# Optimization experiments

Measured on AMD Instinct MI355X. Metric: run time of the kernel, lower is better.

The kernel has to match this reference:

```python
import jax, jax.numpy as jnp
import numpy as np
from jax import lax

VOCAB, EMB, RNN = 20000, 300, 512
B, NCLS, TWORDS = 64, 200, 8


def setup_inputs() -> dict:
    key = jax.random.key(0)
    ks = jax.random.split(key, 10)
    s = 0.05
    return {
        "sentence": jax.random.randint(ks[0], (B, NCLS, TWORDS), 0, VOCAB, dtype=jnp.int32),
        "word2vec": jax.random.normal(ks[1], (VOCAB, EMB), dtype=jnp.float32) * s,
        "W_ih1": jax.random.normal(ks[2], (4 * RNN, EMB), dtype=jnp.float32) * s,
        "W_hh1": jax.random.normal(ks[3], (4 * RNN, RNN), dtype=jnp.float32) * s,
        "b_ih1": jax.random.normal(ks[4], (4 * RNN,), dtype=jnp.float32) * s,
        "b_hh1": jax.random.normal(ks[5], (4 * RNN,), dtype=jnp.float32) * s,
        "W_ih2": jax.random.normal(ks[6], (4 * RNN, RNN), dtype=jnp.float32) * s,
        "W_hh2": jax.random.normal(ks[7], (4 * RNN, RNN), dtype=jnp.float32) * s,
        "b_ih2": jax.random.normal(ks[8], (4 * RNN,), dtype=jnp.float32) * s,
        "b_hh2": jax.random.normal(ks[9], (4 * RNN,), dtype=jnp.float32) * s,
    }


def _lstm_cell(x, h, c, W_ih, W_hh, b):
    # PyTorch LSTMCell gate order: i, f, g, o
    gates = x @ W_ih.T + h @ W_hh.T + b  # [BN, 4*RNN]
    i, f, g, o = jnp.split(gates, 4, axis=-1)
    c_new = jax.nn.sigmoid(f) * c + jax.nn.sigmoid(i) * jnp.tanh(g)
    h_new = jax.nn.sigmoid(o) * jnp.tanh(c_new)
    return h_new, c_new


def reference(sentence, word2vec, W_ih1, W_hh1, b_ih1, b_hh1, W_ih2, W_hh2, b_ih2, b_hh2):
    batch, num_class, max_words = sentence.shape
    bn = batch * num_class
    ids = sentence.reshape(bn, max_words)
    # embedding gather + tanh (dropout is identity in eval mode)
    emb = jnp.tanh(word2vec[ids])              # [BN, T, EMB]
    xs = jnp.swapaxes(emb, 0, 1)               # [T, BN, EMB]
    b1 = b_ih1 + b_hh1
    b2 = b_ih2 + b_hh2
    rnn = W_hh1.shape[1]
    zeros = jnp.zeros((bn, rnn), dtype=word2vec.dtype)
    init = (zeros, zeros, zeros, zeros)

    def step(carry, x):
        h1, c1, h2, c2 = carry
        h1, c1 = _lstm_cell(x, h1, c1, W_ih1, W_hh1, b1)
        h2, c2 = _lstm_cell(h1, h2, c2, W_ih2, W_hh2, b2)
        return (h1, c1, h2, c2), None

    (h1, c1, h2, c2), _ = lax.scan(step, init, xs)
    return h2.reshape(batch, num_class, rnn)
```

## Files before the change

### kernel.cpp

```cpp
#include <hip/hip_runtime.h>
#include <hip/hip_bf16.h>

#define BROWS  12800
#define TSTEPS 8
#define EMB    300
#define EMBP   320
#define RNN    512
#define NG     2048
#define K1     832
#define K2     1024
#define VOCAB  20000

typedef short bf16x8 __attribute__((ext_vector_type(8)));
typedef float f32x4  __attribute__((ext_vector_type(4)));
typedef __hip_bfloat16 bf16;

__device__ __forceinline__ float sigmoidf_(float x) { return 1.f / (1.f + __expf(-x)); }
__device__ __forceinline__ float tanhf_(float x)    { return 1.f - 2.f / (__expf(2.f * x) + 1.f); }

__device__ __forceinline__ void gl_lds16(const bf16* g, bf16* l) {
    __builtin_amdgcn_global_load_lds(
        (const __attribute__((address_space(1))) void*)g,
        (__attribute__((address_space(3))) void*)l,
        16, 0, 0);
}

__global__ void convert_weights(const float* __restrict__ Wih1, const float* __restrict__ Whh1,
                                const float* __restrict__ Wih2, const float* __restrict__ Whh2,
                                const float* __restrict__ bih1, const float* __restrict__ bhh1,
                                const float* __restrict__ bih2, const float* __restrict__ bhh2,
                                bf16* __restrict__ Wc1, bf16* __restrict__ Wc2,
                                float* __restrict__ Bp1, float* __restrict__ Bp2) {
    int idx = blockIdx.x * 256 + threadIdx.x;
    const int n1 = NG * K1;
    const int n2 = NG * K2;
    if (idx < n1) {
        int n = idx / K1, k = idx - n * K1;
        int on = ((n >> 4) & 3) * RNN + (n >> 6) * 16 + (n & 15);
        float v = 0.f;
        if (k < EMB)        v = Wih1[on * EMB + k];
        else if (k >= EMBP) v = Whh1[on * RNN + (k - EMBP)];
        Wc1[idx] = __float2bfloat16(v);
    }
    if (idx < n2) {
        int n = idx >> 10, k = idx & (K2 - 1);
        int on = ((n >> 4) & 3) * RNN + (n >> 6) * 16 + (n & 15);
        float v = (k < RNN) ? Wih2[on * RNN + k] : Whh2[on * RNN + (k - RNN)];
        Wc2[idx] = __float2bfloat16(v);
    }
    if (idx < NG) {
        int on = ((idx >> 4) & 3) * RNN + (idx >> 6) * 16 + (idx & 15);
        Bp1[idx] = bih1[on] + bhh1[on];
        Bp2[idx] = bih2[on] + bhh2[on];
    }
}

__global__ void tanh_w2v(const float* __restrict__ w2v, bf16* __restrict__ W2Vt) {
    int row = blockIdx.x;
    int col = threadIdx.x;
    float v = (col < EMB) ? tanhf_(w2v[row * EMB + col]) : 0.f;
    W2Vt[(size_t)row * EMBP + col] = __float2bfloat16(v);
}

#define BM 128
#define BN 128

__global__ __launch_bounds__(256, 4) void gemm_lstm(
        int role_base, int t,
        const bf16* __restrict__ W2Vt, const int* __restrict__ sent,
        const bf16* __restrict__ Asrc,
        bf16* __restrict__ hdst,
        const bf16* __restrict__ Wc1, const bf16* __restrict__ Wc2,
        const float* __restrict__ Bp1, const float* __restrict__ Bp2,
        float* __restrict__ cst1, float* __restrict__ cst2,
        float* __restrict__ outf, int en_out,
        int Kl1, int Kl2) {
    __shared__ __attribute__((aligned(16))) bf16 sA[BM * 64];
    __shared__ __attribute__((aligned(16))) bf16 sB[BN * 64];

    const int tid  = threadIdx.x;
    const int lane = tid & 63;
    const int wave = tid >> 6;
    const int wm   = wave >> 1, wn = wave & 1;
    const int bn   = blockIdx.x;
    const int bm   = blockIdx.y;
    const int role = blockIdx.z + role_base;

    const bf16*  W;  int ldw, Kl, ksplit, offh;
    const float* Bp; float* cst;
    if (role) { W = Wc1; ldw = K1; Kl = Kl1; ksplit = EMBP; offh = 0;   Bp = Bp1; cst = cst1; }
    else      { W = Wc2; ldw = K2; Kl = Kl2; ksplit = 0;    offh = RNN; Bp = Bp2; cst = cst2; }

    f32x4 acc[4][4];
#pragma unroll
    for (int i = 0; i < 4; ++i)
#pragma unroll
        for (int j = 0; j < 4; ++j)
#pragma unroll
            for (int r = 0; r < 4; ++r) acc[i][j][r] = 0.f;

    const int r = lane & 15, q = lane >> 4;

    int srow[4], scol[4];
#pragma unroll
    for (int c = 0; c < 4; ++c) {
        int ch = c * 256 + tid;
        srow[c] = ch >> 3;
        scol[c] = ((ch & 7) ^ (srow[c] & 7)) * 8;
    }

    int idv[4];
    if (role) {
#pragma unroll
        for (int c = 0; c < 4; ++c)
            idv[c] = sent[(size_t)(bm * BM + srow[c]) * TSTEPS + t];
    }

    const bf16* Wbase = W + (size_t)(bn * BN) * ldw;
    const bf16* Abase = Asrc + (size_t)(bm * BM) * K2;

    for (int kb = 0; kb < Kl; kb += 64) {
        const bool xreg = (kb < ksplit);
#pragma unroll
        for (int c = 0; c < 4; ++c) {
            int ch = c * 256 + tid;
            const bf16* alane = xreg
                ? W2Vt  + (size_t)idv[c] * EMBP + kb + scol[c]
                : Abase + (size_t)srow[c] * K2 + (kb - ksplit) + scol[c];
            gl_lds16(alane, &sA[ch * 8]);
            gl_lds16(Wbase + (size_t)srow[c] * ldw + kb + scol[c], &sB[ch * 8]);
        }
        __syncthreads();
#pragma unroll
        for (int kk = 0; kk < 64; kk += 32) {
            const int kc = kk >> 3;
            bf16x8 af[4], wf[4];
#pragma unroll
            for (int i = 0; i < 4; ++i)
                af[i] = *(const bf16x8*)(&sA[(wm * 64 + i * 16 + r) * 64 + (((q + kc) ^ (r & 7)) * 8)]);
#pragma unroll
            for (int j = 0; j < 4; ++j)
                wf[j] = *(const bf16x8*)(&sB[(wn * 64 + j * 16 + r) * 64 + (((q + kc) ^ (r & 7)) * 8)]);
#pragma unroll
            for (int i = 0; i < 4; ++i)
#pragma unroll
                for (int j = 0; j < 4; ++j)
                    acc[i][j] = __builtin_amdgcn_mfma_f32_16x16x32_bf16(
                        af[i], wf[j], acc[i][j], 0, 0, 0);
        }
        __syncthreads();
    }

    const int colb = bn * BN + wn * 64;
    const int u    = (2 * bn + wn) * 16 + r;
    const float bi = Bp[colb + r];
    const float bf = Bp[colb + 16 + r];
    const float bg = Bp[colb + 32 + r];
    const float bo = Bp[colb + 48 + r];

    float cc[4][4];
#pragma unroll
    for (int i = 0; i < 4; ++i)
#pragma unroll
        for (int rr = 0; rr < 4; ++rr) {
            int row = bm * BM + wm * 64 + i * 16 + q * 4 + rr;
            cc[i][rr] = cst[(size_t)row * RNN + u];
        }

#define HLD 40
#pragma unroll
    for (int i = 0; i < 4; ++i) {
#pragma unroll
        for (int rr = 0; rr < 4; ++rr) {
            int rowl = wm * 64 + i * 16 + q * 4 + rr;
            int row  = bm * BM + rowl;
            size_t cidx = (size_t)row * RNN + u;
            float gi = acc[i][0][rr] + bi;
            float gf = acc[i][1][rr] + bf;
            float gg = acc[i][2][rr] + bg;
            float go = acc[i][3][rr] + bo;
            float cn = sigmoidf_(gf) * cc[i][rr] + sigmoidf_(gi) * tanhf_(gg);
            float h  = sigmoidf_(go) * tanhf_(cn);
            cst[cidx] = cn;
            if (en_out) outf[cidx] = h;
            sA[rowl * HLD + wn * 16 + r] = __float2bfloat16(h);
        }
    }
    __syncthreads();

#pragma unroll
    for (int half = 0; half < 2; ++half) {
        int t2   = half * 256 + tid;
        int rowl = t2 >> 2;
        int c8   = (t2 & 3) * 8;
        uint4 v  = *(const uint4*)&sA[rowl * HLD + c8];
        int row  = bm * BM + rowl;
        int gcol = bn * 32 + c8;
        *(uint4*)&hdst[(size_t)row * K2 + offh + gcol] = v;
    }
#undef HLD
}

extern "C" void kernel_launch(void* const* d_in, const int* in_sizes, int n_in,
                              void* d_out, int out_size, void* d_ws, size_t ws_size,
                              hipStream_t stream) {
    (void)in_sizes; (void)n_in; (void)out_size; (void)ws_size;
    const int*   sent = (const int*)d_in[0];
    const float* w2v  = (const float*)d_in[1];
    const float* Wih1 = (const float*)d_in[2];
    const float* Whh1 = (const float*)d_in[3];
    const float* bih1 = (const float*)d_in[4];
    const float* bhh1 = (const float*)d_in[5];
    const float* Wih2 = (const float*)d_in[6];
    const float* Whh2 = (const float*)d_in[7];
    const float* bih2 = (const float*)d_in[8];
    const float* bhh2 = (const float*)d_in[9];
    float* out = (float*)d_out;

    char* ws = (char*)d_ws;
    float* c1   = (float*)(ws);
    float* c2   = (float*)(ws + 26214400);
    bf16*  A2[2];
    A2[0] = (bf16*)(ws + 52428800);
    A2[1] = (bf16*)(ws + 78643200);
    bf16*  W2Vt = (bf16*) (ws + 104857600);
    bf16*  Wc1  = (bf16*) (ws + 117657600);
    bf16*  Wc2  = (bf16*) (ws + 121065472);
    float* Bp1  = (float*)(ws + 125259776);
    float* Bp2  = (float*)(ws + 125267968);

    hipMemsetAsync(ws, 0, 52428800, stream);

    convert_weights<<<dim3((NG * K2 + 255) / 256), dim3(256), 0, stream>>>(
        Wih1, Whh1, Wih2, Whh2, bih1, bhh1, bih2, bhh2, Wc1, Wc2, Bp1, Bp2);

    tanh_w2v<<<dim3(VOCAB), dim3(EMBP), 0, stream>>>(w2v, W2Vt);

    gemm_lstm<<<dim3(NG / BN, BROWS / BM, 1), dim3(256), 0, stream>>>(
        1, 0, W2Vt, sent,
        A2[1] , A2[0],
        Wc1, Wc2, Bp1, Bp2, c1, c2,
        (float*)nullptr, 0,
        EMBP , 0 );

    for (int s = 1; s <= 7; ++s) {
        gemm_lstm<<<dim3(NG / BN, BROWS / BM, 2), dim3(256), 0, stream>>>(
            0, s, W2Vt, sent,
            A2[(s - 1) & 1], A2[s & 1],
            Wc1, Wc2, Bp1, Bp2, c1, c2,
            (float*)nullptr, 0,
            K1 , (s == 1) ? RNN : K2 );
    }

    gemm_lstm<<<dim3(NG / BN, BROWS / BM, 1), dim3(256), 0, stream>>>(
        0, 0 , W2Vt, sent,
        A2[1], A2[0],
        Wc1, Wc2, Bp1, Bp2, c1, c2,
        out, 1,
        K1 , K2 );
}
```

Before: 1.037 ms.

## Remap blocks XCD-aware, use pointer-increment K loop, skip c-state memset

Workgroup IDs are remapped so that consecutive logical tiles are grouped by raw&7, placing tiles that share weight and activation rows on the same XCD for better L2 reuse. The K loop is split into an embedding-gather phase and a hidden-state phase with running pointers, which removes the per-iteration branch and address recomputation. The 50MB workspace memset is dropped, and the first step of each layer treats the cell state as zero through a flag instead of reading it. The remap relies on the hardcoded grid size of 1600 tiles per role.

New measurement: 1.011 ms. -2.5%, faster.

```diff
diff --git a/kernel.cpp b/kernel.cpp
--- a/kernel.cpp
+++ b/kernel.cpp
@@ -74,7 +74,7 @@
         const float* __restrict__ Bp1, const float* __restrict__ Bp2,
         float* __restrict__ cst1, float* __restrict__ cst2,
         float* __restrict__ outf, int en_out,
-        int Kl1, int Kl2) {
+        int Kl1, int Kl2, int cz1, int cz2) {
     __shared__ __attribute__((aligned(16))) bf16 sA[BM * 64];
     __shared__ __attribute__((aligned(16))) bf16 sB[BN * 64];
 
@@ -82,14 +82,21 @@
     const int lane = tid & 63;
     const int wave = tid >> 6;
     const int wm   = wave >> 1, wn = wave & 1;
-    const int bn   = blockIdx.x;
-    const int bm   = blockIdx.y;
-    const int role = blockIdx.z + role_base;
-
-    const bf16*  W;  int ldw, Kl, ksplit, offh;
+
+    const int zdim  = (int)gridDim.z;
+    const int chunk = (zdim * 1600) >> 3;
+    const int raw   = blockIdx.x + (blockIdx.y << 4) + blockIdx.z * 1600;
+    const int lgc   = (raw & 7) * chunk + (raw >> 3);
+    int role, rem;
+    if (zdim == 2) { role = (lgc >= 1600) ? 1 : 0; rem = lgc - (role ? 1600 : 0); }
+    else           { role = role_base;             rem = lgc; }
+    const int bn = rem & 15;
+    const int bm = rem >> 4;
+
+    const bf16*  W;  int ldw, Kl, ksplit, offh, czero;
     const float* Bp; float* cst;
-    if (role) { W = Wc1; ldw = K1; Kl = Kl1; ksplit = EMBP; offh = 0;   Bp = Bp1; cst = cst1; }
-    else      { W = Wc2; ldw = K2; Kl = Kl2; ksplit = 0;    offh = RNN; Bp = Bp2; cst = cst2; }
+    if (role) { W = Wc1; ldw = K1; Kl = Kl1; ksplit = EMBP; offh = 0;   Bp = Bp1; cst = cst1; czero = cz1; }
+    else      { W = Wc2; ldw = K2; Kl = Kl2; ksplit = 0;    offh = RNN; Bp = Bp2; cst = cst2; czero = cz2; }
 
     f32x4 acc[4][4];
 #pragma unroll
@@ -109,31 +116,37 @@
         scol[c] = ((ch & 7) ^ (srow[c] & 7)) * 8;
     }
 
-    int idv[4];
-    if (role) {
-#pragma unroll
-        for (int c = 0; c < 4; ++c)
-            idv[c] = sent[(size_t)(bm * BM + srow[c]) * TSTEPS + t];
-    }
-
     const bf16* Wbase = W + (size_t)(bn * BN) * ldw;
     const bf16* Abase = Asrc + (size_t)(bm * BM) * K2;
 
-    for (int kb = 0; kb < Kl; kb += 64) {
-        const bool xreg = (kb < ksplit);
+    const bf16* ap[4];
+    const bf16* wp[4];
+#pragma unroll
+    for (int c = 0; c < 4; ++c)
+        wp[c] = Wbase + (size_t)srow[c] * ldw + scol[c];
+    if (role) {
 #pragma unroll
         for (int c = 0; c < 4; ++c) {
-            int ch = c * 256 + tid;
-            const bf16* alane = xreg
-                ? W2Vt  + (size_t)idv[c] * EMBP + kb + scol[c]
-                : Abase + (size_t)srow[c] * K2 + (kb - ksplit) + scol[c];
-            gl_lds16(alane, &sA[ch * 8]);
-            gl_lds16(Wbase + (size_t)srow[c] * ldw + kb + scol[c], &sB[ch * 8]);
+            int id = sent[(size_t)(bm * BM + srow[c]) * TSTEPS + t];
+            ap[c] = W2Vt + (size_t)id * EMBP + scol[c];
+        }
+    } else {
+#pragma unroll
+        for (int c = 0; c < 4; ++c)
+            ap[c] = Abase + (size_t)srow[c] * K2 + scol[c];
+    }
+
+    auto tile = [&]() {
+#pragma unroll
+        for (int c = 0; c < 4; ++c) {
+            gl_lds16(ap[c], &sA[(c * 256 + tid) * 8]);
+            gl_lds16(wp[c], &sB[(c * 256 + tid) * 8]);
+            ap[c] += 64; wp[c] += 64;
         }
         __syncthreads();
 #pragma unroll
-        for (int kk = 0; kk < 64; kk += 32) {
-            const int kc = kk >> 3;
+        for (int kk = 0; kk < 2; ++kk) {
+            const int kc = kk << 2;
             bf16x8 af[4], wf[4];
 #pragma unroll
             for (int i = 0; i < 4; ++i)
@@ -149,7 +162,17 @@
                         af[i], wf[j], acc[i][j], 0, 0, 0);
         }
         __syncthreads();
-    }
+    };
+
+    const int ntx = ksplit >> 6;
+    const int nth = (Kl - ksplit) >> 6;
+    for (int tt = 0; tt < ntx; ++tt) tile();
+    if (role) {
+#pragma unroll
+        for (int c = 0; c < 4; ++c)
+            ap[c] = Abase + (size_t)srow[c] * K2 + scol[c];
+    }
+    for (int tt = 0; tt < nth; ++tt) tile();
 
     const int colb = bn * BN + wn * 64;
     const int u    = (2 * bn + wn) * 16 + r;
@@ -159,13 +182,20 @@
     const float bo = Bp[colb + 48 + r];
 
     float cc[4][4];
-#pragma unroll
-    for (int i = 0; i < 4; ++i)
-#pragma unroll
-        for (int rr = 0; rr < 4; ++rr) {
-            int row = bm * BM + wm * 64 + i * 16 + q * 4 + rr;
-            cc[i][rr] = cst[(size_t)row * RNN + u];
-        }
+    if (czero) {
+#pragma unroll
+        for (int i = 0; i < 4; ++i)
+#pragma unroll
+            for (int rr = 0; rr < 4; ++rr) cc[i][rr] = 0.f;
+    } else {
+#pragma unroll
+        for (int i = 0; i < 4; ++i)
+#pragma unroll
+            for (int rr = 0; rr < 4; ++rr) {
+                int row = bm * BM + wm * 64 + i * 16 + q * 4 + rr;
+                cc[i][rr] = cst[(size_t)row * RNN + u];
+            }
+    }
 
 #define HLD 40
 #pragma unroll
@@ -229,8 +259,6 @@
     float* Bp1  = (float*)(ws + 125259776);
     float* Bp2  = (float*)(ws + 125267968);
 
-    hipMemsetAsync(ws, 0, 52428800, stream);
-
     convert_weights<<<dim3((NG * K2 + 255) / 256), dim3(256), 0, stream>>>(
         Wih1, Whh1, Wih2, Whh2, bih1, bhh1, bih2, bhh2, Wc1, Wc2, Bp1, Bp2);
 
@@ -241,7 +269,7 @@
         A2[1] , A2[0],
         Wc1, Wc2, Bp1, Bp2, c1, c2,
         (float*)nullptr, 0,
-        EMBP , 0 );
+        EMBP , 0 , 1 , 0);
 
     for (int s = 1; s <= 7; ++s) {
         gemm_lstm<<<dim3(NG / BN, BROWS / BM, 2), dim3(256), 0, stream>>>(
@@ -249,7 +277,8 @@
             A2[(s - 1) & 1], A2[s & 1],
             Wc1, Wc2, Bp1, Bp2, c1, c2,
             (float*)nullptr, 0,
-            K1 , (s == 1) ? RNN : K2 );
+            K1 , (s == 1) ? RNN : K2 ,
+            0 , (s == 1) ? 1 : 0 );
     }
 
     gemm_lstm<<<dim3(NG / BN, BROWS / BM, 1), dim3(256), 0, stream>>>(
@@ -257,5 +286,5 @@
         A2[1], A2[0],
         Wc1, Wc2, Bp1, Bp2, c1, c2,
         out, 1,
-        K1 , K2 );
-}
+        K1 , K2 , 0, 0);
+}
```

## Template-specialize LSTM GEMM with unrolled K loop, block swizzle, skip zero cell-state

Applied to the files above, without the earlier changes.

The gemm_lstm kernel is templated on per-role K-tile counts so the K loop is fully unrolled, with precomputed LDS fragment addresses and per-row global pointers. Block indices are remapped by interleaving groups of eight, which reorders how tiles are scheduled and may improve L2 locality. The first step of each layer no longer reads the zero cell state, so the 50MB workspace memset is dropped. The cost is larger code size from the unrolling, and correctness now depends on the czero flags being right for each launch.

Result: faster. 991.1 us (-4.4%).

```diff
diff --git a/kernel.cpp b/kernel.cpp
--- a/kernel.cpp
+++ b/kernel.cpp
@@ -18,12 +18,10 @@
 __device__ __forceinline__ float sigmoidf_(float x) { return 1.f / (1.f + __expf(-x)); }
 __device__ __forceinline__ float tanhf_(float x)    { return 1.f - 2.f / (__expf(2.f * x) + 1.f); }
 
-__device__ __forceinline__ void gl_lds16(const bf16* g, bf16* l) {
-    __builtin_amdgcn_global_load_lds(
-        (const __attribute__((address_space(1))) void*)g,
-        (__attribute__((address_space(3))) void*)l,
-        16, 0, 0);
-}
+#define GL16(p, l)                                                          \
+    __builtin_amdgcn_global_load_lds(                                       \
+        (const __attribute__((address_space(1))) void*)(p),                 \
+        (__attribute__((address_space(3))) void*)(l), 16, 0, 0)
 
 __global__ void convert_weights(const float* __restrict__ Wih1, const float* __restrict__ Whh1,
                                 const float* __restrict__ Wih2, const float* __restrict__ Whh2,
@@ -65,16 +63,52 @@
 #define BM 128
 #define BN 128
 
+#define STAGE8(AP, AE, WE) do {                                             \
+    GL16(AP[0] + (AE), &sA[(0 * 256 + tid) * 8]);                           \
+    GL16(AP[1] + (AE), &sA[(1 * 256 + tid) * 8]);                           \
+    GL16(AP[2] + (AE), &sA[(2 * 256 + tid) * 8]);                           \
+    GL16(AP[3] + (AE), &sA[(3 * 256 + tid) * 8]);                           \
+    GL16(wp[0] + (WE), &sB[(0 * 256 + tid) * 8]);                           \
+    GL16(wp[1] + (WE), &sB[(1 * 256 + tid) * 8]);                           \
+    GL16(wp[2] + (WE), &sB[(2 * 256 + tid) * 8]);                           \
+    GL16(wp[3] + (WE), &sB[(3 * 256 + tid) * 8]);                           \
+} while (0)
+
+#define COMPUTE() do {                                                      \
+    __syncthreads();                                                        \
+    _Pragma("unroll")                                                       \
+    for (int kk = 0; kk < 2; ++kk) {                                        \
+        bf16x8 af[4], wf[4];                                                \
+        _Pragma("unroll")                                                   \
+        for (int i = 0; i < 4; ++i)                                         \
+            af[i] = *(const bf16x8*)(adA[kk] + i * 1024);                   \
+        _Pragma("unroll")                                                   \
+        for (int j = 0; j < 4; ++j)                                         \
+            wf[j] = *(const bf16x8*)(adB[kk] + j * 1024);                   \
+        _Pragma("unroll")                                                   \
+        for (int i = 0; i < 4; ++i)                                         \
+            _Pragma("unroll")                                               \
+            for (int j = 0; j < 4; ++j)                                     \
+                acc[i][j] = __builtin_amdgcn_mfma_f32_16x16x32_bf16(        \
+                    af[i], wf[j], acc[i][j], 0, 0, 0);                      \
+    }                                                                       \
+    __syncthreads();                                                        \
+} while (0)
+
+#define XT(n)  do { STAGE8(xp, (n) * 64, (n) * 64); COMPUTE(); } while (0)
+#define HT1(n) do { STAGE8(hp, (n) * 64, (5 + (n)) * 64); COMPUTE(); } while (0)
+#define HT2(n) do { STAGE8(hp, (n) * 64, (n) * 64); COMPUTE(); } while (0)
+
+template<int NTH1, int NTL2, int ZM>
 __global__ __launch_bounds__(256, 4) void gemm_lstm(
-        int role_base, int t,
+        int t,
         const bf16* __restrict__ W2Vt, const int* __restrict__ sent,
         const bf16* __restrict__ Asrc,
         bf16* __restrict__ hdst,
         const bf16* __restrict__ Wc1, const bf16* __restrict__ Wc2,
         const float* __restrict__ Bp1, const float* __restrict__ Bp2,
         float* __restrict__ cst1, float* __restrict__ cst2,
-        float* __restrict__ outf, int en_out,
-        int Kl1, int Kl2) {
+        float* __restrict__ outf, int en_out, int cz1, int cz2) {
     __shared__ __attribute__((aligned(16))) bf16 sA[BM * 64];
     __shared__ __attribute__((aligned(16))) bf16 sB[BN * 64];
 
@@ -82,14 +116,25 @@
     const int lane = tid & 63;
     const int wave = tid >> 6;
     const int wm   = wave >> 1, wn = wave & 1;
-    const int bn   = blockIdx.x;
-    const int bm   = blockIdx.y;
-    const int role = blockIdx.z + role_base;
-
-    const bf16*  W;  int ldw, Kl, ksplit, offh;
+
+    int role, rem;
+    if (ZM == 0) {
+        const int raw = blockIdx.x + (blockIdx.y << 4) + blockIdx.z * 1600;
+        const int lgc = (raw & 7) * 400 + (raw >> 3);
+        role = (lgc >= 1600) ? 1 : 0;
+        rem  = lgc - (role ? 1600 : 0);
+    } else {
+        const int raw = blockIdx.x + (blockIdx.y << 4);
+        rem  = (raw & 7) * 200 + (raw >> 3);
+        role = (ZM == 1) ? 1 : 0;
+    }
+    const int bn = rem & 15;
+    const int bm = rem >> 4;
+
+    const bf16*  W;  int ldw, offh, czero;
     const float* Bp; float* cst;
-    if (role) { W = Wc1; ldw = K1; Kl = Kl1; ksplit = EMBP; offh = 0;   Bp = Bp1; cst = cst1; }
-    else      { W = Wc2; ldw = K2; Kl = Kl2; ksplit = 0;    offh = RNN; Bp = Bp2; cst = cst2; }
+    if (role) { W = Wc1; ldw = K1; offh = 0;   Bp = Bp1; cst = cst1; czero = cz1; }
+    else      { W = Wc2; ldw = K2; offh = RNN; Bp = Bp2; cst = cst2; czero = cz2; }
 
     f32x4 acc[4][4];
 #pragma unroll
@@ -97,7 +142,7 @@
 #pragma unroll
         for (int j = 0; j < 4; ++j)
 #pragma unroll
-            for (int r = 0; r < 4; ++r) acc[i][j][r] = 0.f;
+            for (int rr = 0; rr < 4; ++rr) acc[i][j][rr] = 0.f;
 
     const int r = lane & 15, q = lane >> 4;
 
@@ -109,46 +154,46 @@
         scol[c] = ((ch & 7) ^ (srow[c] & 7)) * 8;
     }
 
-    int idv[4];
-    if (role) {
+    const bf16* adA[2];
+    const bf16* adB[2];
+#pragma unroll
+    for (int kk = 0; kk < 2; ++kk) {
+        int x = ((q + 4 * kk) ^ (r & 7)) * 8;
+        adA[kk] = &sA[(wm * 64 + r) * 64 + x];
+        adB[kk] = &sB[(wn * 64 + r) * 64 + x];
+    }
+
+    const bf16* wp[4];
+#pragma unroll
+    for (int c = 0; c < 4; ++c)
+        wp[c] = W + (size_t)(bn * BN + srow[c]) * ldw + scol[c];
+
+    if (ZM == 1 || (ZM == 0 && role)) {
+        {
+            const bf16* xp[4];
+#pragma unroll
+            for (int c = 0; c < 4; ++c) {
+                int id = sent[(bm * BM + srow[c]) * TSTEPS + t];
+                xp[c] = W2Vt + (size_t)id * EMBP + scol[c];
+            }
+            XT(0); XT(1); XT(2); XT(3); XT(4);
+        }
+        if (NTH1 > 0) {
+            const bf16* hp[4];
+#pragma unroll
+            for (int c = 0; c < 4; ++c)
+                hp[c] = Asrc + (size_t)(bm * BM + srow[c]) * K2 + scol[c];
+            HT1(0); HT1(1); HT1(2); HT1(3); HT1(4); HT1(5); HT1(6); HT1(7);
+        }
+    } else {
+        const bf16* hp[4];
 #pragma unroll
         for (int c = 0; c < 4; ++c)
-            idv[c] = sent[(size_t)(bm * BM + srow[c]) * TSTEPS + t];
-    }
-
-    const bf16* Wbase = W + (size_t)(bn * BN) * ldw;
-    const bf16* Abase = Asrc + (size_t)(bm * BM) * K2;
-
-    for (int kb = 0; kb < Kl; kb += 64) {
-        const bool xreg = (kb < ksplit);
-#pragma unroll
-        for (int c = 0; c < 4; ++c) {
-            int ch = c * 256 + tid;
-            const bf16* alane = xreg
-                ? W2Vt  + (size_t)idv[c] * EMBP + kb + scol[c]
-                : Abase + (size_t)srow[c] * K2 + (kb - ksplit) + scol[c];
-            gl_lds16(alane, &sA[ch * 8]);
-            gl_lds16(Wbase + (size_t)srow[c] * ldw + kb + scol[c], &sB[ch * 8]);
+            hp[c] = Asrc + (size_t)(bm * BM + srow[c]) * K2 + scol[c];
+        HT2(0); HT2(1); HT2(2); HT2(3); HT2(4); HT2(5); HT2(6); HT2(7);
+        if (NTL2 == 16) {
+            HT2(8); HT2(9); HT2(10); HT2(11); HT2(12); HT2(13); HT2(14); HT2(15);
         }
-        __syncthreads();
-#pragma unroll
-        for (int kk = 0; kk < 64; kk += 32) {
-            const int kc = kk >> 3;
-            bf16x8 af[4], wf[4];
-#pragma unroll
-            for (int i = 0; i < 4; ++i)
-                af[i] = *(const bf16x8*)(&sA[(wm * 64 + i * 16 + r) * 64 + (((q + kc) ^ (r & 7)) * 8)]);
-#pragma unroll
-            for (int j = 0; j < 4; ++j)
-                wf[j] = *(const bf16x8*)(&sB[(wn * 64 + j * 16 + r) * 64 + (((q + kc) ^ (r & 7)) * 8)]);
-#pragma unroll
-            for (int i = 0; i < 4; ++i)
-#pragma unroll
-                for (int j = 0; j < 4; ++j)
-                    acc[i][j] = __builtin_amdgcn_mfma_f32_16x16x32_bf16(
-                        af[i], wf[j], acc[i][j], 0, 0, 0);
-        }
-        __syncthreads();
     }
 
     const int colb = bn * BN + wn * 64;
@@ -159,13 +204,20 @@
     const float bo = Bp[colb + 48 + r];
 
     float cc[4][4];
-#pragma unroll
-    for (int i = 0; i < 4; ++i)
-#pragma unroll
-        for (int rr = 0; rr < 4; ++rr) {
-            int row = bm * BM + wm * 64 + i * 16 + q * 4 + rr;
-            cc[i][rr] = cst[(size_t)row * RNN + u];
-        }
+    if (czero) {
+#pragma unroll
+        for (int i = 0; i < 4; ++i)
+#pragma unroll
+            for (int rr = 0; rr < 4; ++rr) cc[i][rr] = 0.f;
+    } else {
+#pragma unroll
+        for (int i = 0; i < 4; ++i)
+#pragma unroll
+            for (int rr = 0; rr < 4; ++rr) {
+                int row = bm * BM + wm * 64 + i * 16 + q * 4 + rr;
+                cc[i][rr] = cst[(size_t)row * RNN + u];
+            }
+    }
 
 #define HLD 40
 #pragma unroll
@@ -229,33 +281,34 @@
     float* Bp1  = (float*)(ws + 125259776);
     float* Bp2  = (float*)(ws + 125267968);
 
-    hipMemsetAsync(ws, 0, 52428800, stream);
-
     convert_weights<<<dim3((NG * K2 + 255) / 256), dim3(256), 0, stream>>>(
         Wih1, Whh1, Wih2, Whh2, bih1, bhh1, bih2, bhh2, Wc1, Wc2, Bp1, Bp2);
 
     tanh_w2v<<<dim3(VOCAB), dim3(EMBP), 0, stream>>>(w2v, W2Vt);
 
-    gemm_lstm<<<dim3(NG / BN, BROWS / BM, 1), dim3(256), 0, stream>>>(
-        1, 0, W2Vt, sent,
-        A2[1] , A2[0],
+    const dim3 blk(256);
+    const dim3 g1(NG / BN, BROWS / BM, 1);
+    const dim3 g2(NG / BN, BROWS / BM, 2);
+
+    gemm_lstm<0, 0, 1><<<g1, blk, 0, stream>>>(
+        0, W2Vt, sent, A2[1] , A2[0],
         Wc1, Wc2, Bp1, Bp2, c1, c2,
-        (float*)nullptr, 0,
-        EMBP , 0 );
-
-    for (int s = 1; s <= 7; ++s) {
-        gemm_lstm<<<dim3(NG / BN, BROWS / BM, 2), dim3(256), 0, stream>>>(
-            0, s, W2Vt, sent,
-            A2[(s - 1) & 1], A2[s & 1],
+        (float*)nullptr, 0, 1 , 0);
+
+    gemm_lstm<8, 8, 0><<<g2, blk, 0, stream>>>(
+        1, W2Vt, sent, A2[0], A2[1],
+        Wc1, Wc2, Bp1, Bp2, c1, c2,
+        (float*)nullptr, 0, 0, 1 );
+
+    for (int s = 2; s <= 7; ++s) {
+        gemm_lstm<8, 16, 0><<<g2, blk, 0, stream>>>(
+            s, W2Vt, sent, A2[(s - 1) & 1], A2[s & 1],
             Wc1, Wc2, Bp1, Bp2, c1, c2,
-            (float*)nullptr, 0,
-            K1 , (s == 1) ? RNN : K2 );
-    }
-
-    gemm_lstm<<<dim3(NG / BN, BROWS / BM, 1), dim3(256), 0, stream>>>(
-        0, 0 , W2Vt, sent,
-        A2[1], A2[0],
+            (float*)nullptr, 0, 0, 0);
+    }
+
+    gemm_lstm<0, 16, 2><<<g1, blk, 0, stream>>>(
+        0, W2Vt, sent, A2[1], A2[0],
         Wc1, Wc2, Bp1, Bp2, c1, c2,
-        out, 1,
-        K1 , K2 );
+        out, 1, 0, 0);
 }
```
